# Performance work log

Hardware: AMD Instinct MI355X
Metric: run time of the kernel (lower is better)

## Reference

```python
import jax, jax.numpy as jnp
import numpy as np
from jax import lax

B, N, C = 256, 128, 256
GRID_SIZE = 0.05
# eta/phi are sampled in [0, 2), so (v - min)/0.05 < 40 -> grid index <= 39.
# Using a static 40x40 grid is mathematically identical to the dynamic
# H = max+1, W = max+1 of the original: extra rows/cols are zero, which
# matches the 'same' zero padding the depthwise conv would see anyway,
# and gathered positions are unchanged.
HMAX, WMAX = 40, 40
KH = KW = 3


def setup_inputs() -> dict:
    key = jax.random.key(0)
    ks = jax.random.split(key, 9)
    x = jax.random.normal(ks[0], (B, N, C), jnp.float32)
    eta = jax.random.uniform(ks[1], (B, N), jnp.float32, 0.0, 2.0)
    phi = jax.random.uniform(ks[2], (B, N), jnp.float32, 0.0, 2.0)
    # depthwise conv kernel, HWIO with I = in_channels/groups = 1
    conv_kernel = jax.random.normal(ks[3], (KH, KW, 1, C), jnp.float32) * 0.1
    conv_bias = jax.random.normal(ks[4], (C,), jnp.float32) * 0.01
    dense_w = jax.random.normal(ks[5], (C, C), jnp.float32) * (1.0 / np.sqrt(C))
    dense_b = jax.random.normal(ks[6], (C,), jnp.float32) * 0.01
    gamma = jnp.ones((C,), jnp.float32)
    beta = jnp.zeros((C,), jnp.float32)
    return {
        "x": x, "eta": eta, "phi": phi,
        "conv_kernel": conv_kernel, "conv_bias": conv_bias,
        "dense_w": dense_w, "dense_b": dense_b,
        "gamma": gamma, "beta": beta,
    }


def reference(x, eta, phi, conv_kernel, conv_bias, dense_w, dense_b, gamma, beta):
    Bq, Nq, Cq = x.shape
    # quantize particle positions to grid bins (per-batch min shift)
    ge = ((eta - eta.min(axis=1, keepdims=True)) / GRID_SIZE).astype(jnp.int32)  # [B,N]
    gp = ((phi - phi.min(axis=1, keepdims=True)) / GRID_SIZE).astype(jnp.int32)  # [B,N]
    b_idx = jnp.arange(Bq)[:, None]  # broadcasts against [B,N]

    # scatter-add particle features into dense (eta,phi) grid
    grid = jnp.zeros((Bq, HMAX, WMAX, Cq), x.dtype).at[b_idx, ge, gp].add(x)

    # depthwise 3x3 conv, 'same' zero padding, per-channel bias
    grid = lax.conv_general_dilated(
        grid, conv_kernel, window_strides=(1, 1), padding="SAME",
        dimension_numbers=("NHWC", "HWIO", "NHWC"), feature_group_count=Cq,
    ) + conv_bias

    # gather back to particles
    out = grid[b_idx, ge, gp]  # [B, N, C]

    # pointwise dense
    out = jnp.einsum("bnc,cd->bnd", out, dense_w) + dense_b

    # layer norm (eps=1e-6, biased variance, channel affine)
    mean = out.mean(axis=-1, keepdims=True)
    var = jnp.mean(jnp.square(out - mean), axis=-1, keepdims=True)
    out = (out - mean) * lax.rsqrt(var + 1e-6) * gamma + beta

    return x + out
```

## Files before the change

kernel.cpp:

```cpp
#include <hip/hip_runtime.h>

typedef __attribute__((ext_vector_type(8))) short bf16x8;
typedef __attribute__((ext_vector_type(4))) float f32x4;

#define Bq 256
#define Nq 128
#define Cq 256
#define TP 16
#define NBLK (Nq / TP)

__device__ __forceinline__ unsigned short f2bf(float f) {
    unsigned int u = __float_as_uint(f);
    u += 0x7fffu + ((u >> 16) & 1u);
    return (unsigned short)(u >> 16);
}

__global__ __launch_bounds__(256) void wpack_kernel(const float* __restrict__ dw,
                                                    unsigned short* __restrict__ wp) {
    int tid = blockIdx.x * 256 + threadIdx.x;
    int j    = tid & 7;
    int lane = (tid >> 3) & 63;
    int nt   = (tid >> 9) & 15;
    int kt   = tid >> 13;
    int k = kt * 32 + (lane >> 4) * 8 + j;
    int n = nt * 16 + (lane & 15);
    wp[tid] = f2bf(dw[k * Cq + n]);
}

__global__ __launch_bounds__(256, 5) void fused_kernel(
    const float* __restrict__ x, const float* __restrict__ eta, const float* __restrict__ phi,
    const float* __restrict__ ck, const float* __restrict__ cb,
    const unsigned short* __restrict__ wp, const float* __restrict__ db,
    const float* __restrict__ gamma, const float* __restrict__ beta,
    float* __restrict__ out) {
    const int b  = blockIdx.x >> 3;
    const int p0 = (blockIdx.x & (NBLK - 1)) * TP;
    const int t  = threadIdx.x;
    const int lane = t & 63, wave = t >> 6;

    __shared__ int   s_ge[Nq], s_gp[Nq];
    __shared__ float s_ck[9 * Cq];
    __shared__ float s_min[4];
    __shared__ int   s_cnt[TP];
    __shared__ int   s_list[TP][Nq];
    __shared__ unsigned short s_A[8 * 64 * 8];
    __shared__ float s_sum[TP][4], s_sq[TP][4];

    float ev = 0.f, pv = 0.f;
    if (t < Nq) {
        ev = eta[b * Nq + t];
        pv = phi[b * Nq + t];
        float emin = ev, pmin = pv;
#pragma unroll
        for (int off = 32; off > 0; off >>= 1) {
            emin = fminf(emin, __shfl_down(emin, off));
            pmin = fminf(pmin, __shfl_down(pmin, off));
        }
        if ((t & 63) == 0) { s_min[wave] = emin; s_min[2 + wave] = pmin; }
    }
#pragma unroll
    for (int i = t; i < 9 * Cq; i += 256) s_ck[i] = ck[i];
    if (t < TP) s_cnt[t] = 0;
    __syncthreads();

    if (t < Nq) {
        float Emin = fminf(s_min[0], s_min[1]);
        float Pmin = fminf(s_min[2], s_min[3]);
        s_ge[t] = (int)((ev - Emin) / 0.05f);
        s_gp[t] = (int)((pv - Pmin) / 0.05f);
    }
    __syncthreads();

    {
        int pp = t >> 4, sub = t & 15;
        int th = s_ge[p0 + pp], tw = s_gp[p0 + pp];
#pragma unroll
        for (int i = 0; i < 8; ++i) {
            int m = sub * 8 + i;
            int dh = s_ge[m] - th, dv = s_gp[m] - tw;
            if (dh >= -1 && dh <= 1 && dv >= -1 && dv <= 1) {
                int k = (dh + 1) * 3 + (dv + 1);
                int pos = atomicAdd(&s_cnt[pp], 1);
                s_list[pp][pos] = ((k * Cq) << 16) | (m * Cq);
            }
        }
    }
    __syncthreads();

    {
        const int c = t;
        const float bias_c = cb[c];
        const int kt = c >> 5, g = (c >> 3) & 3, jj = c & 7;
        const float* xb = x + (size_t)b * Nq * Cq + c;
        for (int pp = 0; pp < TP; ++pp) {
            float acc = bias_c;
            int cnt = s_cnt[pp];
            const int* lst = s_list[pp];
            for (int i = 0; i < cnt; ++i) {
                int e = lst[i];
                acc += s_ck[(e >> 16) + c] * xb[e & 0xffff];
            }
            int lidx = ((pp + 2 * g) & 15) | (g << 4);
            s_A[(kt * 64 + lidx) * 8 + jj] = f2bf(acc);
        }
    }
    __syncthreads();

    f32x4 acc[4];
#pragma unroll
    for (int ntl = 0; ntl < 4; ++ntl) acc[ntl] = (f32x4){0.f, 0.f, 0.f, 0.f};

    const int g2 = lane >> 4, m2 = lane & 15;
    const int alidx = ((m2 + 2 * g2) & 15) | (g2 << 4);
#pragma unroll
    for (int kt2 = 0; kt2 < 8; ++kt2) {
        bf16x8 af = *reinterpret_cast<const bf16x8*>(&s_A[(kt2 * 64 + alidx) * 8]);
#pragma unroll
        for (int ntl = 0; ntl < 4; ++ntl) {
            int nt = wave * 4 + ntl;
            bf16x8 bfr = *reinterpret_cast<const bf16x8*>(&wp[((kt2 * 16 + nt) * 64 + lane) * 8]);
            acc[ntl] = __builtin_amdgcn_mfma_f32_16x16x32_bf16(af, bfr, acc[ntl], 0, 0, 0);
        }
    }

    float dbv[4], gv[4], bv[4];
#pragma unroll
    for (int ntl = 0; ntl < 4; ++ntl) {
        int col = (wave * 4 + ntl) * 16 + m2;
        dbv[ntl] = db[col]; gv[ntl] = gamma[col]; bv[ntl] = beta[col];
    }
#pragma unroll
    for (int r = 0; r < 4; ++r) {
        float a = 0.f, q = 0.f;
#pragma unroll
        for (int ntl = 0; ntl < 4; ++ntl) {
            float y = acc[ntl][r] + dbv[ntl];
            a += y; q += y * y;
        }
#pragma unroll
        for (int off = 8; off >= 1; off >>= 1) {
            a += __shfl_xor(a, off);
            q += __shfl_xor(q, off);
        }
        if (m2 == 0) {
            int row = g2 * 4 + r;
            s_sum[row][wave] = a;
            s_sq[row][wave]  = q;
        }
    }
    __syncthreads();

#pragma unroll
    for (int r = 0; r < 4; ++r) {
        int row = g2 * 4 + r;
        float s = s_sum[row][0] + s_sum[row][1] + s_sum[row][2] + s_sum[row][3];
        float q = s_sq[row][0] + s_sq[row][1] + s_sq[row][2] + s_sq[row][3];
        float mean = s * (1.0f / Cq);
        float var  = q * (1.0f / Cq) - mean * mean;
        float inv  = rsqrtf(var + 1e-6f);
        int gbase = (b * Nq + p0 + row) * Cq + wave * 64 + m2;
#pragma unroll
        for (int ntl = 0; ntl < 4; ++ntl) {
            float y = acc[ntl][r] + dbv[ntl];
            int idx = gbase + ntl * 16;
            out[idx] = x[idx] + (y - mean) * inv * gv[ntl] + bv[ntl];
        }
    }
}

extern "C" void kernel_launch(void* const* d_in, const int* in_sizes, int n_in,
                              void* d_out, int out_size, void* d_ws, size_t ws_size,
                              hipStream_t stream) {
    const float* x     = (const float*)d_in[0];
    const float* eta   = (const float*)d_in[1];
    const float* phi   = (const float*)d_in[2];
    const float* ck    = (const float*)d_in[3];
    const float* cb    = (const float*)d_in[4];
    const float* dw    = (const float*)d_in[5];
    const float* db    = (const float*)d_in[6];
    const float* gamma = (const float*)d_in[7];
    const float* beta  = (const float*)d_in[8];
    float* out = (float*)d_out;

    unsigned short* wpk = (unsigned short*)d_ws;

    wpack_kernel<<<Cq, 256, 0, stream>>>(dw, wpk);
    fused_kernel<<<Bq * NBLK, 256, 0, stream>>>(x, eta, phi, ck, cb, wpk, db,
                                                gamma, beta, out);
}
```

Before: 130.4 us.

## Parallelize conv gather over particles with float4 channel vectors

The depthwise-conv gather stage is restructured so each thread owns one target particle and a group of 16 channels using float4 loads. Previously each thread handled one channel and looped serially over all 16 particles. Neighbor lists are packed into 16-bit entries and padded to even length with a zeroed dummy kernel slot, so the inner loop processes two neighbors per iteration. Launch bounds drop the occupancy hint from 5 to 4, trading occupancy for more registers to hold the vector accumulators and loads.

```diff
diff --git a/kernel.cpp b/kernel.cpp
--- a/kernel.cpp
+++ b/kernel.cpp
@@ -13,6 +13,15 @@
     unsigned int u = __float_as_uint(f);
     u += 0x7fffu + ((u >> 16) & 1u);
     return (unsigned short)(u >> 16);
+}
+
+struct ushort4_t { unsigned short x, y, z, w; };
+
+__device__ __forceinline__ void fma4(float4& a, const float4& k, const float4& x) {
+    a.x = fmaf(k.x, x.x, a.x);
+    a.y = fmaf(k.y, x.y, a.y);
+    a.z = fmaf(k.z, x.z, a.z);
+    a.w = fmaf(k.w, x.w, a.w);
 }
 
 __global__ __launch_bounds__(256) void wpack_kernel(const float* __restrict__ dw,
@@ -27,7 +36,7 @@
     wp[tid] = f2bf(dw[k * Cq + n]);
 }
 
-__global__ __launch_bounds__(256, 5) void fused_kernel(
+__global__ __launch_bounds__(256, 4) void fused_kernel(
     const float* __restrict__ x, const float* __restrict__ eta, const float* __restrict__ phi,
     const float* __restrict__ ck, const float* __restrict__ cb,
     const unsigned short* __restrict__ wp, const float* __restrict__ db,
@@ -39,11 +48,11 @@
     const int lane = t & 63, wave = t >> 6;
 
     __shared__ int   s_ge[Nq], s_gp[Nq];
-    __shared__ float s_ck[9 * Cq];
+    __shared__ float s_ck[10 * Cq];
     __shared__ float s_min[4];
     __shared__ int   s_cnt[TP];
-    __shared__ int   s_list[TP][Nq];
-    __shared__ unsigned short s_A[8 * 64 * 8];
+    __shared__ unsigned short s_list[TP][132];
+    __shared__ unsigned short s_A[8 * 64 * 8] __attribute__((aligned(16)));
     __shared__ float s_sum[TP][4], s_sq[TP][4];
 
     float ev = 0.f, pv = 0.f;
@@ -60,6 +69,7 @@
     }
 #pragma unroll
     for (int i = t; i < 9 * Cq; i += 256) s_ck[i] = ck[i];
+    s_ck[9 * Cq + t] = 0.0f;
     if (t < TP) s_cnt[t] = 0;
     __syncthreads();
 
@@ -71,37 +81,63 @@
     }
     __syncthreads();
 
+    const int pp = t >> 4, cg = t & 15;
+
     {
-        int pp = t >> 4, sub = t & 15;
         int th = s_ge[p0 + pp], tw = s_gp[p0 + pp];
 #pragma unroll
         for (int i = 0; i < 8; ++i) {
-            int m = sub * 8 + i;
+            int m = cg * 8 + i;
             int dh = s_ge[m] - th, dv = s_gp[m] - tw;
             if (dh >= -1 && dh <= 1 && dv >= -1 && dv <= 1) {
                 int k = (dh + 1) * 3 + (dv + 1);
                 int pos = atomicAdd(&s_cnt[pp], 1);
-                s_list[pp][pos] = ((k * Cq) << 16) | (m * Cq);
+                s_list[pp][pos] = (unsigned short)(m | (k << 7));
             }
         }
     }
     __syncthreads();
+    if (t < TP) {
+        int c = s_cnt[t];
+        if (c & 1) { s_list[t][c] = (unsigned short)(9 << 7); s_cnt[t] = c + 1; }
+    }
+    __syncthreads();
 
     {
-        const int c = t;
-        const float bias_c = cb[c];
-        const int kt = c >> 5, g = (c >> 3) & 3, jj = c & 7;
-        const float* xb = x + (size_t)b * Nq * Cq + c;
-        for (int pp = 0; pp < TP; ++pp) {
-            float acc = bias_c;
-            int cnt = s_cnt[pp];
-            const int* lst = s_list[pp];
-            for (int i = 0; i < cnt; ++i) {
-                int e = lst[i];
-                acc += s_ck[(e >> 16) + c] * xb[e & 0xffff];
-            }
-            int lidx = ((pp + 2 * g) & 15) | (g << 4);
-            s_A[(kt * 64 + lidx) * 8 + jj] = f2bf(acc);
+        const float4* x4  = (const float4*)x + (size_t)b * (Nq * Cq / 4) + cg;
+        const float4* ck4 = (const float4*)s_ck + cg;
+        const float4* cb4 = (const float4*)cb + cg;
+        float4 a0 = cb4[0], a1 = cb4[16], a2 = cb4[32], a3 = cb4[48];
+
+        const int cnt = s_cnt[pp];
+        const unsigned short* lst = s_list[pp];
+        for (int i = 0; i < cnt; i += 2) {
+            int e0 = lst[i], e1 = lst[i + 1];
+            const float4* xp0 = x4  + ((e0 & 127) << 6);
+            const float4* kp0 = ck4 + ((e0 >> 7)  << 6);
+            const float4* xp1 = x4  + ((e1 & 127) << 6);
+            const float4* kp1 = ck4 + ((e1 >> 7)  << 6);
+            float4 X00 = xp0[0], X01 = xp0[16], X02 = xp0[32], X03 = xp0[48];
+            float4 X10 = xp1[0], X11 = xp1[16], X12 = xp1[32], X13 = xp1[48];
+            float4 K00 = kp0[0], K01 = kp0[16], K02 = kp0[32], K03 = kp0[48];
+            float4 K10 = kp1[0], K11 = kp1[16], K12 = kp1[32], K13 = kp1[48];
+            fma4(a0, K00, X00); fma4(a1, K01, X01);
+            fma4(a2, K02, X02); fma4(a3, K03, X03);
+            fma4(a0, K10, X10); fma4(a1, K11, X11);
+            fma4(a2, K12, X12); fma4(a3, K13, X13);
+        }
+
+        const int g = (cg >> 1) & 3;
+        const int lidx = ((pp + 2 * g) & 15) | (g << 4);
+        const int off = (cg & 1) * 4;
+        float4 aj[4] = {a0, a1, a2, a3};
+#pragma unroll
+        for (int j = 0; j < 4; ++j) {
+            int kt = j * 2 + (cg >> 3);
+            ushort4_t v;
+            v.x = f2bf(aj[j].x); v.y = f2bf(aj[j].y);
+            v.z = f2bf(aj[j].z); v.w = f2bf(aj[j].w);
+            *(ushort4_t*)&s_A[(kt * 64 + lidx) * 8 + off] = v;
         }
     }
     __syncthreads();
```

Result: faster. 119.5 us (-8.3%).
